# Optimization experiments

Hardware: AMD Instinct MI355X
Metric: run time of the kernel (lower is better)

Reference implementation:

```python
import jax, jax.numpy as jnp
import numpy as np

N, T, VN, C = 64, 512, 10, 128
HEADS, DH = 8, 16
INNER = HEADS * DH  # 128
BN_EPS = 1e-5


def _build_mask():
    # depth == 0 graph: facial-region connections + self links, symmetric 10x10
    m = np.zeros((VN, VN), dtype=np.float32)
    conn = [[0, 1], [0, 2], [2, 1], [3, 4], [3, 5], [4, 5],
            [6, 7], [6, 8], [6, 9], [8, 7], [9, 7], [8, 9]]
    for a, b in conn:
        m[a, b] = 1.0
        m[b, a] = 1.0
    for i in range(VN):
        m[i, i] = 1.0
    return jnp.asarray(m)


def setup_inputs() -> dict:
    key = jax.random.key(0)
    k = jax.random.split(key, 6)
    x = jax.random.normal(k[0], (N, T, VN, C), dtype=jnp.float32)
    gamma = 1.0 + 0.02 * jax.random.normal(k[1], (C,), dtype=jnp.float32)
    beta = 0.02 * jax.random.normal(k[2], (C,), dtype=jnp.float32)
    w_qkv = 0.02 * jax.random.normal(k[3], (C, 3 * INNER), dtype=jnp.float32)
    w_out = 0.02 * jax.random.normal(k[4], (INNER, C), dtype=jnp.float32)
    b_out = 0.02 * jax.random.normal(k[5], (C,), dtype=jnp.float32)
    return {"x": x, "gamma": gamma, "beta": beta, "w_qkv": w_qkv,
            "w_out": w_out, "b_out": b_out, "mask": _build_mask()}


def reference(x, gamma, beta, w_qkv, w_out, b_out, mask):
    n, t, vn, c = x.shape
    xb = x.reshape(-1, vn, c)                     # (b, vn, c), b = n*t
    # BatchNorm1d over channel c (training mode: batch stats over b and vn)
    mean = jnp.mean(xb, axis=(0, 1))
    var = jnp.var(xb, axis=(0, 1))                # biased, matches torch BN
    y = (xb - mean) * jax.lax.rsqrt(var + BN_EPS) * gamma + beta
    # fused QKV projection (Linear, no bias)
    qkv = y @ w_qkv                               # (b, vn, 3*inner)
    q, k, v = jnp.split(qkv, 3, axis=-1)
    split_heads = lambda z: z.reshape(-1, vn, HEADS, DH).transpose(0, 2, 1, 3)
    q, k, v = split_heads(q), split_heads(k), split_heads(v)  # (b, h, vn, dh)
    scale = DH ** -0.5
    dots = jnp.einsum('bhid,bhjd->bhij', q, k) * scale
    dots = dots * mask                            # multiplicative graph mask
    attn = jax.nn.softmax(dots, axis=-1)
    out = jnp.einsum('bhij,bhjd->bhid', attn, v)  # (b, h, vn, dh)
    out = out.transpose(0, 2, 1, 3).reshape(-1, vn, INNER)
    out = out @ w_out + b_out                     # output projection
    return out.reshape(n, t, vn, c)
```

## Files before the change

kernel.cpp:

```cpp
#include <hip/hip_runtime.h>


#define VNODES 10
#define CH 128
#define ROWS_TOTAL 327680
#define G 4
#define MROWS 40
#define MT 3
#define SX 136

typedef __bf16 bf16x8 __attribute__((ext_vector_type(8)));
typedef float f32x4 __attribute__((ext_vector_type(4)));
typedef unsigned u32x4 __attribute__((ext_vector_type(4)));

__device__ __forceinline__ unsigned short f2bf(float f) {
    unsigned u = __float_as_uint(f);
    u += 0x7fffu + ((u >> 16) & 1u);
    return (unsigned short)(u >> 16);
}

__global__ __launch_bounds__(256) void stats_kernel(
        const float* __restrict__ x,
        float* __restrict__ ws_sum, float* __restrict__ ws_sq) {
    __shared__ float lsum[8][128];
    __shared__ float lsq[8][128];
    int t = threadIdx.x;
    int slot = t >> 5, g = t & 31;
    float s[4], q[4];
#pragma unroll
    for (int k = 0; k < 4; ++k) { s[k] = 0.f; q[k] = 0.f; }
    size_t base_row = (size_t)blockIdx.x * 160;
    for (int p = 0; p < 20; ++p) {
        size_t row = base_row + p * 8 + slot;
        f32x4 v = *(const f32x4*)(x + row * CH + g * 4);
#pragma unroll
        for (int k = 0; k < 4; ++k) {
            s[k] += v[k];
            q[k] = fmaf(v[k], v[k], q[k]);
        }
    }
#pragma unroll
    for (int k = 0; k < 4; ++k) { lsum[slot][g * 4 + k] = s[k]; lsq[slot][g * 4 + k] = q[k]; }
    __syncthreads();
    if (t < 128) {
        float ts = 0.f, tq = 0.f;
#pragma unroll
        for (int sl = 0; sl < 8; ++sl) { ts += lsum[sl][t]; tq += lsq[sl][t]; }
        atomicAdd(&ws_sum[t], ts);
        atomicAdd(&ws_sq[t], tq);
    }
}

__global__ __launch_bounds__(256) void prep_kernel(
        const float* __restrict__ wqkv, const float* __restrict__ wout,
        const float* __restrict__ gamma, const float* __restrict__ beta,
        const float* __restrict__ stats,
        unsigned short* __restrict__ fq, unsigned short* __restrict__ fo,
        float* __restrict__ bq) {
    __shared__ float sh_s[128];
    if (blockIdx.x < 32) {
        int tid = blockIdx.x * 256 + threadIdx.x;
        if (tid < 24 * 4 * 64) {
            int l = tid & 63;
            int kt = (tid >> 6) & 3;
            int nt = tid >> 8;
            int quad = l >> 4, n = l & 15;
#pragma unroll
            for (int j = 0; j < 8; ++j) {
                int k = kt * 32 + quad * 8 + j;
                float mean = stats[k] * (1.0f / ROWS_TOTAL);
                float var = stats[128 + k] * (1.0f / ROWS_TOTAL) - mean * mean;
                float sc = gamma[k] * rsqrtf(var + 1e-5f);
                fq[tid * 8 + j] = f2bf(sc * wqkv[k * 384 + nt * 16 + n]);
            }
        } else if (tid < 24 * 4 * 64 + 8 * 4 * 64) {
            int u = tid - 24 * 4 * 64;
            int l = u & 63;
            int kt = (u >> 6) & 3;
            int nt = u >> 8;
            int quad = l >> 4, n = l & 15;
#pragma unroll
            for (int j = 0; j < 8; ++j) {
                int k = kt * 32 + quad * 8 + j;
                fo[u * 8 + j] = f2bf(wout[k * 128 + nt * 16 + n]);
            }
        }
    } else {
        int t = threadIdx.x;
        if (t < 128) {
            float mean = stats[t] * (1.0f / ROWS_TOTAL);
            float var = stats[128 + t] * (1.0f / ROWS_TOTAL) - mean * mean;
            float sc = gamma[t] * rsqrtf(var + 1e-5f);
            sh_s[t] = beta[t] - mean * sc;
        }
        __syncthreads();
        for (int n = t; n < 384; n += 256) {
            float acc = 0.f;
#pragma unroll 8
            for (int c = 0; c < 128; ++c) acc = fmaf(sh_s[c], wqkv[c * 384 + n], acc);
            bq[n] = acc;
        }
    }
}

__global__ __launch_bounds__(512, 6) void main_kernel(
        const float* __restrict__ x,
        const float* __restrict__ maskp,
        const float* __restrict__ bq,
        const unsigned short* __restrict__ wqkv_f,
        const unsigned short* __restrict__ wout_f,
        const float* __restrict__ b_out,
        float* __restrict__ out) {
    __shared__ __align__(16) unsigned short xT[48 * SX];
    __shared__ __align__(16) unsigned short qT[40 * SX];
    __shared__ __align__(16) unsigned short kTb[40 * SX];
    __shared__ __align__(16) unsigned short vTb[40 * SX];
    __shared__ float bq_s[384], bout_s[128], mask_s[VNODES * VNODES];

    int tid = threadIdx.x;
    int lane = tid & 63, w = tid >> 6;
    size_t row0 = (size_t)blockIdx.x * MROWS;

    if (tid < 384) bq_s[tid] = bq[tid];
    else bout_s[tid - 384] = b_out[tid - 384];
    if (tid < VNODES * VNODES) mask_s[tid] = maskp[tid];
    {
        int r = 40 + (tid >> 6), c = (tid & 63) * 2;
        *(unsigned*)(xT + r * SX + c) = 0u;
    }

    {
#pragma unroll
        for (int p = 0; p < 3; ++p) {
            int idx = p * 512 + tid;
            if (idx < 1280) {
                int r = idx >> 5, g = idx & 31;
                f32x4 v = *(const f32x4*)(x + (row0 + r) * CH + g * 4);
                unsigned short o0 = f2bf(v[0]), o1 = f2bf(v[1]);
                unsigned short o2 = f2bf(v[2]), o3 = f2bf(v[3]);
                unsigned two0 = (unsigned)o0 | ((unsigned)o1 << 16);
                unsigned two1 = (unsigned)o2 | ((unsigned)o3 << 16);
                *(unsigned*)(xT + r * SX + g * 4) = two0;
                *(unsigned*)(xT + r * SX + g * 4 + 2) = two1;
            }
        }
    }
    __syncthreads();

    {
        bf16x8 bf[3][4];
#pragma unroll
        for (int ni = 0; ni < 3; ++ni) {
            int nt = w + ni * 8;
#pragma unroll
            for (int kt = 0; kt < 4; ++kt)
                bf[ni][kt] = *(const bf16x8*)(wqkv_f + ((nt * 4 + kt) * 64 + lane) * 8);
        }
        int l15 = lane & 15, quad = lane >> 4;
        for (int mt = 0; mt < MT; ++mt) {
            bf16x8 a[4];
#pragma unroll
            for (int kt = 0; kt < 4; ++kt)
                a[kt] = *(const bf16x8*)(xT + (mt * 16 + l15) * SX + kt * 32 + quad * 8);
            f32x4 accq = {0.f,0.f,0.f,0.f}, acck = {0.f,0.f,0.f,0.f}, accv = {0.f,0.f,0.f,0.f};
#pragma unroll
            for (int kt = 0; kt < 4; ++kt) {
                accq = __builtin_amdgcn_mfma_f32_16x16x32_bf16(a[kt], bf[0][kt], accq, 0, 0, 0);
                acck = __builtin_amdgcn_mfma_f32_16x16x32_bf16(a[kt], bf[1][kt], acck, 0, 0, 0);
                accv = __builtin_amdgcn_mfma_f32_16x16x32_bf16(a[kt], bf[2][kt], accv, 0, 0, 0);
            }
            int col = w * 16 + l15;
            float bqq = bq_s[col], bqk = bq_s[128 + col], bqv = bq_s[256 + col];
#pragma unroll
            for (int i = 0; i < 4; ++i) {
                int rr = mt * 16 + quad * 4 + i;
                if (rr < MROWS) {
                    qT[rr * SX + col]  = f2bf(accq[i] + bqq);
                    kTb[rr * SX + col] = f2bf(acck[i] + bqk);
                    vTb[rr * SX + col] = f2bf(accv[i] + bqv);
                }
            }
        }
    }
    __syncthreads();

    if (tid < G * 8 * VNODES) {
        int h = tid / (G * VNODES);
        int rem = tid - h * (G * VNODES);
        int b = rem / VNODES;
        int i = rem - b * VNODES;
        int rowi = b * VNODES + i;
        const unsigned* qp = (const unsigned*)(qT + rowi * SX + h * 16);
        u32x4 qw0 = *(const u32x4*)qp;
        u32x4 qw1 = *(const u32x4*)(qp + 4);
        float qv[16];
#pragma unroll
        for (int d = 0; d < 4; ++d) {
            qv[2*d]     = __uint_as_float(qw0[d] << 16);
            qv[2*d+1]   = __uint_as_float(qw0[d] & 0xffff0000u);
            qv[8+2*d]   = __uint_as_float(qw1[d] << 16);
            qv[8+2*d+1] = __uint_as_float(qw1[d] & 0xffff0000u);
        }
        float p[VNODES];
        float mx = -1e30f;
#pragma unroll
        for (int j = 0; j < VNODES; ++j) {
            const unsigned* kp = (const unsigned*)(kTb + (b * VNODES + j) * SX + h * 16);
            u32x4 k0 = *(const u32x4*)kp;
            u32x4 k1 = *(const u32x4*)(kp + 4);
            float dot = 0.f;
#pragma unroll
            for (int d = 0; d < 4; ++d) {
                dot = fmaf(qv[2*d],     __uint_as_float(k0[d] << 16), dot);
                dot = fmaf(qv[2*d+1],   __uint_as_float(k0[d] & 0xffff0000u), dot);
                dot = fmaf(qv[8+2*d],   __uint_as_float(k1[d] << 16), dot);
                dot = fmaf(qv[8+2*d+1], __uint_as_float(k1[d] & 0xffff0000u), dot);
            }
            p[j] = dot * 0.25f * mask_s[i * VNODES + j];
            mx = fmaxf(mx, p[j]);
        }
        float s = 0.f;
#pragma unroll
        for (int j = 0; j < VNODES; ++j) { p[j] = __expf(p[j] - mx); s += p[j]; }
        float inv = 1.0f / s;
        float o[16];
#pragma unroll
        for (int d = 0; d < 16; ++d) o[d] = 0.f;
#pragma unroll
        for (int j = 0; j < VNODES; ++j) {
            const unsigned* vp = (const unsigned*)(vTb + (b * VNODES + j) * SX + h * 16);
            u32x4 v0 = *(const u32x4*)vp;
            u32x4 v1 = *(const u32x4*)(vp + 4);
#pragma unroll
            for (int d = 0; d < 4; ++d) {
                o[2*d]     = fmaf(p[j], __uint_as_float(v0[d] << 16), o[2*d]);
                o[2*d+1]   = fmaf(p[j], __uint_as_float(v0[d] & 0xffff0000u), o[2*d+1]);
                o[8+2*d]   = fmaf(p[j], __uint_as_float(v1[d] << 16), o[8+2*d]);
                o[8+2*d+1] = fmaf(p[j], __uint_as_float(v1[d] & 0xffff0000u), o[8+2*d+1]);
            }
        }
#pragma unroll
        for (int d2 = 0; d2 < 8; ++d2) {
            unsigned ow = (unsigned)f2bf(o[d2 * 2] * inv)
                        | ((unsigned)f2bf(o[d2 * 2 + 1] * inv) << 16);
            *(unsigned*)(xT + rowi * SX + h * 16 + d2 * 2) = ow;
        }
    }
    __syncthreads();

    {
        bf16x8 bfw[4];
#pragma unroll
        for (int kt = 0; kt < 4; ++kt)
            bfw[kt] = *(const bf16x8*)(wout_f + ((w * 4 + kt) * 64 + lane) * 8);
        int l15 = lane & 15, quad = lane >> 4;
        int col = w * 16 + l15;
        float bias = bout_s[col];
        for (int mt = 0; mt < MT; ++mt) {
            f32x4 acc = {0.f, 0.f, 0.f, 0.f};
#pragma unroll
            for (int kt = 0; kt < 4; ++kt) {
                bf16x8 a = *(const bf16x8*)(xT + (mt * 16 + l15) * SX + kt * 32 + quad * 8);
                acc = __builtin_amdgcn_mfma_f32_16x16x32_bf16(a, bfw[kt], acc, 0, 0, 0);
            }
#pragma unroll
            for (int i = 0; i < 4; ++i) {
                int rr = mt * 16 + quad * 4 + i;
                if (rr < MROWS) out[(row0 + rr) * CH + col] = acc[i] + bias;
            }
        }
    }
}

extern "C" void kernel_launch(void* const* d_in, const int* in_sizes, int n_in,
                              void* d_out, int out_size, void* d_ws, size_t ws_size,
                              hipStream_t stream) {
    const float* x     = (const float*)d_in[0];
    const float* gamma = (const float*)d_in[1];
    const float* beta  = (const float*)d_in[2];
    const float* wqkv  = (const float*)d_in[3];
    const float* wout  = (const float*)d_in[4];
    const float* bout  = (const float*)d_in[5];
    const float* maskp = (const float*)d_in[6];
    float* out = (float*)d_out;

    char* ws = (char*)d_ws;
    float* ws_stats = (float*)ws;
    float* bq = (float*)(ws + 1024);
    unsigned short* fq = (unsigned short*)(ws + 4096);
    unsigned short* fo = (unsigned short*)(ws + 4096 + 98304);

    hipMemsetAsync(ws, 0, 1024, stream);
    stats_kernel<<<2048, 256, 0, stream>>>(x, ws_stats, ws_stats + 128);
    prep_kernel<<<33, 256, 0, stream>>>(wqkv, wout, gamma, beta, ws_stats, fq, fo, bq);
    main_kernel<<<8192, 512, 0, stream>>>(x, maskp, bq, fq, fo, bout, out);
}
```

Measured before the change: 426.4 us.

## Stage output through LDS for coalesced stores, use hardware bf16 converts and packed FMAs

The output projection results now go to a shared-memory tile, which reuses the merged K/V buffer, and are then written to global memory as coalesced 16-byte vector stores instead of scattered scalar stores. The manual round-to-nearest bf16 conversion is replaced with native __bf16 casts and paired conversions. The attention dot products and weighted sums use 2-wide packed FMAs. The softmax scale is folded into Q when Q is written. This adds one barrier and reuses LDS, and the packed reductions change summation order slightly.

```diff
diff --git a/kernel.cpp b/kernel.cpp
--- a/kernel.cpp
+++ b/kernel.cpp
@@ -8,15 +8,30 @@
 #define MROWS 40
 #define MT 3
 #define SX 136
+#define SK 132
 
 typedef __bf16 bf16x8 __attribute__((ext_vector_type(8)));
+typedef __bf16 bf16x2 __attribute__((ext_vector_type(2)));
 typedef float f32x4 __attribute__((ext_vector_type(4)));
+typedef float f32x2 __attribute__((ext_vector_type(2)));
 typedef unsigned u32x4 __attribute__((ext_vector_type(4)));
-
-__device__ __forceinline__ unsigned short f2bf(float f) {
-    unsigned u = __float_as_uint(f);
-    u += 0x7fffu + ((u >> 16) & 1u);
-    return (unsigned short)(u >> 16);
+typedef unsigned u32x2 __attribute__((ext_vector_type(2)));
+
+__device__ __forceinline__ unsigned short f2bfu(float f) {
+    __bf16 h = (__bf16)f;
+    return __builtin_bit_cast(unsigned short, h);
+}
+__device__ __forceinline__ unsigned packcvt(float a, float b) {
+    bf16x2 t;
+    t[0] = (__bf16)a;
+    t[1] = (__bf16)b;
+    return __builtin_bit_cast(unsigned, t);
+}
+__device__ __forceinline__ f32x2 up2(unsigned u) {
+    f32x2 r;
+    r[0] = __uint_as_float(u << 16);
+    r[1] = __uint_as_float(u & 0xffff0000u);
+    return r;
 }
 
 __global__ __launch_bounds__(256) void stats_kernel(
@@ -71,7 +86,7 @@
                 float mean = stats[k] * (1.0f / ROWS_TOTAL);
                 float var = stats[128 + k] * (1.0f / ROWS_TOTAL) - mean * mean;
                 float sc = gamma[k] * rsqrtf(var + 1e-5f);
-                fq[tid * 8 + j] = f2bf(sc * wqkv[k * 384 + nt * 16 + n]);
+                fq[tid * 8 + j] = f2bfu(sc * wqkv[k * 384 + nt * 16 + n]);
             }
         } else if (tid < 24 * 4 * 64 + 8 * 4 * 64) {
             int u = tid - 24 * 4 * 64;
@@ -82,7 +97,7 @@
 #pragma unroll
             for (int j = 0; j < 8; ++j) {
                 int k = kt * 32 + quad * 8 + j;
-                fo[u * 8 + j] = f2bf(wout[k * 128 + nt * 16 + n]);
+                fo[u * 8 + j] = f2bfu(wout[k * 128 + nt * 16 + n]);
             }
         }
     } else {
@@ -113,9 +128,12 @@
         float* __restrict__ out) {
     __shared__ __align__(16) unsigned short xT[48 * SX];
     __shared__ __align__(16) unsigned short qT[40 * SX];
-    __shared__ __align__(16) unsigned short kTb[40 * SX];
-    __shared__ __align__(16) unsigned short vTb[40 * SX];
+    __shared__ __align__(16) unsigned short kvT[80 * SX];
     __shared__ float bq_s[384], bout_s[128], mask_s[VNODES * VNODES];
+
+    unsigned short* kTb = kvT;
+    unsigned short* vTb = kvT + 40 * SX;
+    float* oT = (float*)kvT;
 
     int tid = threadIdx.x;
     int lane = tid & 63, w = tid >> 6;
@@ -136,12 +154,10 @@
             if (idx < 1280) {
                 int r = idx >> 5, g = idx & 31;
                 f32x4 v = *(const f32x4*)(x + (row0 + r) * CH + g * 4);
-                unsigned short o0 = f2bf(v[0]), o1 = f2bf(v[1]);
-                unsigned short o2 = f2bf(v[2]), o3 = f2bf(v[3]);
-                unsigned two0 = (unsigned)o0 | ((unsigned)o1 << 16);
-                unsigned two1 = (unsigned)o2 | ((unsigned)o3 << 16);
-                *(unsigned*)(xT + r * SX + g * 4) = two0;
-                *(unsigned*)(xT + r * SX + g * 4 + 2) = two1;
+                u32x2 two;
+                two[0] = packcvt(v[0], v[1]);
+                two[1] = packcvt(v[2], v[3]);
+                *(u32x2*)(xT + r * SX + g * 4) = two;
             }
         }
     }
@@ -175,9 +191,9 @@
             for (int i = 0; i < 4; ++i) {
                 int rr = mt * 16 + quad * 4 + i;
                 if (rr < MROWS) {
-                    qT[rr * SX + col]  = f2bf(accq[i] + bqq);
-                    kTb[rr * SX + col] = f2bf(acck[i] + bqk);
-                    vTb[rr * SX + col] = f2bf(accv[i] + bqv);
+                    qT[rr * SX + col]  = f2bfu((accq[i] + bqq) * 0.25f);
+                    kTb[rr * SX + col] = f2bfu(acck[i] + bqk);
+                    vTb[rr * SX + col] = f2bfu(accv[i] + bqv);
                 }
             }
         }
@@ -193,13 +209,11 @@
         const unsigned* qp = (const unsigned*)(qT + rowi * SX + h * 16);
         u32x4 qw0 = *(const u32x4*)qp;
         u32x4 qw1 = *(const u32x4*)(qp + 4);
-        float qv[16];
+        f32x2 qv[8];
 #pragma unroll
         for (int d = 0; d < 4; ++d) {
-            qv[2*d]     = __uint_as_float(qw0[d] << 16);
-            qv[2*d+1]   = __uint_as_float(qw0[d] & 0xffff0000u);
-            qv[8+2*d]   = __uint_as_float(qw1[d] << 16);
-            qv[8+2*d+1] = __uint_as_float(qw1[d] & 0xffff0000u);
+            qv[d]     = up2(qw0[d]);
+            qv[4 + d] = up2(qw1[d]);
         }
         float p[VNODES];
         float mx = -1e30f;
@@ -208,42 +222,39 @@
             const unsigned* kp = (const unsigned*)(kTb + (b * VNODES + j) * SX + h * 16);
             u32x4 k0 = *(const u32x4*)kp;
             u32x4 k1 = *(const u32x4*)(kp + 4);
-            float dot = 0.f;
+            f32x2 acc2 = {0.f, 0.f};
 #pragma unroll
             for (int d = 0; d < 4; ++d) {
-                dot = fmaf(qv[2*d],     __uint_as_float(k0[d] << 16), dot);
-                dot = fmaf(qv[2*d+1],   __uint_as_float(k0[d] & 0xffff0000u), dot);
-                dot = fmaf(qv[8+2*d],   __uint_as_float(k1[d] << 16), dot);
-                dot = fmaf(qv[8+2*d+1], __uint_as_float(k1[d] & 0xffff0000u), dot);
-            }
-            p[j] = dot * 0.25f * mask_s[i * VNODES + j];
+                acc2 = __builtin_elementwise_fma(qv[d],     up2(k0[d]), acc2);
+                acc2 = __builtin_elementwise_fma(qv[4 + d], up2(k1[d]), acc2);
+            }
+            p[j] = (acc2[0] + acc2[1]) * mask_s[i * VNODES + j];
             mx = fmaxf(mx, p[j]);
         }
         float s = 0.f;
 #pragma unroll
         for (int j = 0; j < VNODES; ++j) { p[j] = __expf(p[j] - mx); s += p[j]; }
         float inv = 1.0f / s;
-        float o[16];
-#pragma unroll
-        for (int d = 0; d < 16; ++d) o[d] = 0.f;
+        f32x2 o2[8];
+#pragma unroll
+        for (int d = 0; d < 8; ++d) o2[d] = (f32x2){0.f, 0.f};
 #pragma unroll
         for (int j = 0; j < VNODES; ++j) {
             const unsigned* vp = (const unsigned*)(vTb + (b * VNODES + j) * SX + h * 16);
             u32x4 v0 = *(const u32x4*)vp;
             u32x4 v1 = *(const u32x4*)(vp + 4);
+            f32x2 pp = {p[j], p[j]};
 #pragma unroll
             for (int d = 0; d < 4; ++d) {
-                o[2*d]     = fmaf(p[j], __uint_as_float(v0[d] << 16), o[2*d]);
-                o[2*d+1]   = fmaf(p[j], __uint_as_float(v0[d] & 0xffff0000u), o[2*d+1]);
-                o[8+2*d]   = fmaf(p[j], __uint_as_float(v1[d] << 16), o[8+2*d]);
-                o[8+2*d+1] = fmaf(p[j], __uint_as_float(v1[d] & 0xffff0000u), o[8+2*d+1]);
-            }
-        }
+                o2[d]     = __builtin_elementwise_fma(pp, up2(v0[d]), o2[d]);
+                o2[4 + d] = __builtin_elementwise_fma(pp, up2(v1[d]), o2[4 + d]);
+            }
+        }
+        f32x2 iv = {inv, inv};
 #pragma unroll
         for (int d2 = 0; d2 < 8; ++d2) {
-            unsigned ow = (unsigned)f2bf(o[d2 * 2] * inv)
-                        | ((unsigned)f2bf(o[d2 * 2 + 1] * inv) << 16);
-            *(unsigned*)(xT + rowi * SX + h * 16 + d2 * 2) = ow;
+            f32x2 r = o2[d2] * iv;
+            *(unsigned*)(xT + rowi * SX + h * 16 + d2 * 2) = packcvt(r[0], r[1]);
         }
     }
     __syncthreads();
@@ -266,7 +277,19 @@
 #pragma unroll
             for (int i = 0; i < 4; ++i) {
                 int rr = mt * 16 + quad * 4 + i;
-                if (rr < MROWS) out[(row0 + rr) * CH + col] = acc[i] + bias;
+                if (rr < MROWS) oT[rr * SK + col] = acc[i] + bias;
+            }
+        }
+    }
+    __syncthreads();
+
+    {
+#pragma unroll
+        for (int p = 0; p < 3; ++p) {
+            int idx = p * 512 + tid;
+            if (idx < 1280) {
+                int r = idx >> 5, g = idx & 31;
+                *(f32x4*)(out + (row0 + r) * CH + g * 4) = *(const f32x4*)(oT + r * SK + g * 4);
             }
         }
     }
```

Measured after the change: 443.9 us. 4.1% more time.
